# Optimization experiments

Hardware: AMD Instinct MI355X
Metric: run time of the kernel (lower is better)

## Reference

```python
import jax, jax.numpy as jnp
import numpy as np

ROPE_BASE = 10000.0


def _rope(x):
    # x: (B, S, H, D) -- rotate-half RoPE applied per head over the sequence dim
    B, S, H, D = x.shape
    half = D // 2
    inv_freq = 1.0 / (ROPE_BASE ** (jnp.arange(half, dtype=jnp.float32) / half))
    ang = jnp.arange(S, dtype=jnp.float32)[:, None] * inv_freq[None, :]  # (S, half)
    cos = jnp.cos(ang)[None, :, None, :].astype(x.dtype)
    sin = jnp.sin(ang)[None, :, None, :].astype(x.dtype)
    x1, x2 = x[..., :half], x[..., half:]
    return jnp.concatenate([x1 * cos - x2 * sin, x2 * cos + x1 * sin], axis=-1)


def setup_inputs() -> dict:
    key = jax.random.key(0)
    ks = jax.random.split(key, 7)
    B, S, D = 8, 1024, 512
    HD = 512  # num_heads * key_dim = 8 * 64
    scale = 0.02
    return {
        "query": jax.random.normal(ks[0], (B, S, D), dtype=jnp.float32),
        "value": jax.random.normal(ks[1], (B, S, D), dtype=jnp.float32),
        "key_in": jax.random.normal(ks[2], (B, S, D), dtype=jnp.float32),
        "Wq": jax.random.normal(ks[3], (D, HD), dtype=jnp.float32) * scale,
        "Wk": jax.random.normal(ks[4], (D, HD), dtype=jnp.float32) * scale,
        "Wv": jax.random.normal(ks[5], (D, HD), dtype=jnp.float32) * scale,
        "Wo": jax.random.normal(ks[6], (HD, D), dtype=jnp.float32) * scale,
    }


def reference(query, value, key_in, Wq, Wk, Wv, Wo):
    H, Dh = 8, 64
    B, Sq, _ = query.shape
    Sk = key_in.shape[1]
    # QKV projections, split heads: (B, S, H, Dh)
    q = (query @ Wq).reshape(B, Sq, H, Dh)
    v = (value @ Wv).reshape(B, Sk, H, Dh)
    k = (key_in @ Wk).reshape(B, Sk, H, Dh)
    # inline RoPE on q and k (applied before head transpose, as in the original)
    q = _rope(q)
    k = _rope(k)
    # scaled dot-product attention with causal mask
    q = q * (1.0 / jnp.sqrt(jnp.asarray(Dh, q.dtype)))
    scores = jnp.einsum("bqhd,bkhd->bhqk", q, k)  # (B, H, Sq, Sk)
    causal = jnp.tril(jnp.ones((Sq, Sk), dtype=bool))[None, None]
    scores = jnp.where(causal, scores, jnp.asarray(-1e9, scores.dtype))
    probs = jax.nn.softmax(scores, axis=-1)
    out = jnp.einsum("bhqk,bkhd->bqhd", probs, v)  # (B, Sq, H, Dh)
    out = out.reshape(B, Sq, H * Dh) @ Wo  # output projection
    return out
```

## Files before the change

kernel.cpp:

```cpp
#include <hip/hip_runtime.h>
#include <hip/hip_bf16.h>
#include <stdint.h>

#define DEV static __device__ __forceinline__

typedef __attribute__((ext_vector_type(8)))  short    s16x8;
typedef __attribute__((ext_vector_type(4)))  short    s16x4;
typedef __attribute__((ext_vector_type(8)))  __bf16   bf16x8;
typedef __attribute__((ext_vector_type(2)))  __bf16   bf16x2;
typedef __attribute__((ext_vector_type(4)))  float    f32x4;
typedef __attribute__((ext_vector_type(16))) float    f32x16;
typedef __attribute__((ext_vector_type(2)))  unsigned u32x2;
typedef __attribute__((ext_vector_type(4)))  unsigned u32x4;

DEV short f2b(float f){
  union{float f; uint32_t i;} x; x.f = f;
  uint32_t r = x.i + 0x7FFFu + ((x.i >> 16) & 1u);
  return (short)(r >> 16);
}
DEV unsigned packbf(float a, float b){
  bf16x2 v = { (__bf16)a, (__bf16)b };
  return __builtin_bit_cast(unsigned, v);
}
DEV bf16x8 as_bf(s16x8 v){ return __builtin_bit_cast(bf16x8, v); }
DEV float fexp2(float x){ return __builtin_amdgcn_exp2f(x); }
DEV f32x4 mf(s16x8 a, s16x8 b, f32x4 c){
  return __builtin_amdgcn_mfma_f32_16x16x32_bf16(as_bf(a), as_bf(b), c, 0, 0, 0);
}
DEV f32x16 mf32(s16x8 a, s16x8 b, f32x16 c){
  return __builtin_amdgcn_mfma_f32_32x32x16_bf16(as_bf(a), as_bf(b), c, 0, 0, 0);
}

DEV void gload_lds16(const void* g, void* l){
  __builtin_amdgcn_global_load_lds((const __attribute__((address_space(1))) void*)g,
                                   (__attribute__((address_space(3))) void*)l, 16, 0, 0);
}

#if __has_builtin(__builtin_amdgcn_permlane32_swap)
DEV void pswap2(unsigned a, unsigned b, unsigned& x, unsigned& y){
  u32x2 rr = __builtin_amdgcn_permlane32_swap(a, b, false, false);
  x = rr[0]; y = rr[1];
}
DEV float partner32(float v, int hi){
  unsigned u = __builtin_bit_cast(unsigned, v);
  u32x2 rr = __builtin_amdgcn_permlane32_swap(u, u, false, false);
  return __builtin_bit_cast(float, hi ? rr[0] : rr[1]);
}
#else
DEV void pswap2(unsigned a, unsigned b, unsigned& x, unsigned& y){
  unsigned pa_ = (unsigned)__shfl_xor((int)a, 32, 64);
  unsigned pb_ = (unsigned)__shfl_xor((int)b, 32, 64);
  int lo = ((threadIdx.x & 63) < 32);
  x = lo ? a   : pb_;
  y = lo ? pa_ : b;
}
DEV float partner32(float v, int hi){ (void)hi; return __shfl_xor(v, 32, 64); }
#endif

__global__ __launch_bounds__(256) void k_conv3(const float* __restrict__ q,
                                               const float* __restrict__ k,
                                               const float* __restrict__ v,
                                               short* __restrict__ out){
  int z = blockIdx.z;
  const float* in = (z == 0) ? q : (z == 1) ? k : v;
  int i = (blockIdx.x * 256 + threadIdx.x) * 4;
  float4 val = *(const float4*)(in + i);
  short o[4] = { f2b(val.x), f2b(val.y), f2b(val.z), f2b(val.w) };
  *(uint2*)(out + (size_t)z * 4194304 + i) = *(uint2*)o;
}

__global__ __launch_bounds__(256) void k_wt4(const float* __restrict__ w0,
                                             const float* __restrict__ w1,
                                             const float* __restrict__ w2,
                                             const float* __restrict__ w3,
                                             short* __restrict__ wt){
  __shared__ float tile[32][33];
  int z = blockIdx.z;
  const float* w = (z == 0) ? w0 : (z == 1) ? w1 : (z == 2) ? w2 : w3;
  short* o = wt + (size_t)z * 262144;
  int bx = blockIdx.x * 32, by = blockIdx.y * 32;
  int tx = threadIdx.x, ty = threadIdx.y;
  for (int j = 0; j < 32; j += 8)
    tile[ty + j][tx] = w[(size_t)(by + ty + j) * 512 + bx + tx];
  __syncthreads();
  for (int j = 0; j < 32; j += 8)
    o[(size_t)(bx + ty + j) * 512 + by + tx] = f2b(tile[tx][ty + j]);
}

__global__ __launch_bounds__(256) void k_table(float* __restrict__ tab){
  int idx = blockIdx.x * 256 + threadIdx.x;
  int s = idx >> 5, j = idx & 31;
  float inv = __expf(-(float)j * (1.0f / 32.0f) * logf(10000.0f));
  float ang = (float)s * inv;
  tab[idx * 2 + 0] = cosf(ang);
  tab[idx * 2 + 1] = sinf(ang);
}

__global__ __launch_bounds__(256) void k_qkv(const short* __restrict__ Xb,
                                             const short* __restrict__ Wcat,
                                             const float* __restrict__ tab,
                                             short* __restrict__ Qa,
                                             short* __restrict__ Ka,
                                             short* __restrict__ Vt){
  __shared__ __align__(16) short Al[2][4096];
  __shared__ __align__(16) short Bl[2][4096];
  const int t = threadIdx.x, w = t >> 6, lane = t & 63, fr = lane & 15, fg = lane >> 4;
  const int sel = blockIdx.y >> 2;
  const short* X = Xb + (size_t)sel * 4194304;
  const int bm = blockIdx.x * 128, bn = blockIdx.y * 128;
  const int wm = (w >> 1) * 64, wn = (w & 1) * 64;

  auto stage = [&](int buf, int k0){
#pragma unroll
    for (int q = 0; q < 2; q++){
      int lin = q * 256 + t;
      int row = lin >> 2, sl = lin & 3;
      int gs = (sl ^ (row & 3)) * 8;
      gload_lds16(X    + (size_t)(bm + row) * 512 + k0 + gs, &Al[buf][(q * 256 + w * 64) * 8]);
      gload_lds16(Wcat + (size_t)(bn + row) * 512 + k0 + gs, &Bl[buf][(q * 256 + w * 64) * 8]);
    }
  };

  f32x4 acc[4][4] = {};
  stage(0, 0);
  __syncthreads();
  int cur = 0;
  for (int t16 = 0; t16 < 16; ++t16){
    if (t16 < 15) stage(cur ^ 1, (t16 + 1) * 32);
    s16x8 af[4], bv[4];
#pragma unroll
    for (int f = 0; f < 4; f++){
      int ra = wm + f * 16 + fr;
      af[f] = *(const s16x8*)(&Al[cur][ra * 32 + ((fg ^ (ra & 3)) * 8)]);
      int rb = wn + f * 16 + fr;
      bv[f] = *(const s16x8*)(&Bl[cur][rb * 32 + ((fg ^ (rb & 3)) * 8)]);
    }
#pragma unroll
    for (int i = 0; i < 4; i++)
#pragma unroll
      for (int jj = 0; jj < 4; jj++)
        acc[i][jj] = mf(af[i], bv[jj], acc[i][jj]);
    __syncthreads();
    cur ^= 1;
  }

  const int row0 = bm + wm + fg * 4;
  const int b = row0 >> 10;
  const int s_base = row0 & 1023;
  const int hh = (((blockIdx.y & 3) * 128) + wn) >> 6;
  if (sel < 2){
    const float scale = (sel == 0) ? 0.125f * 1.44269504f : 1.0f;
    short* out = (sel == 0) ? Qa : Ka;
#pragma unroll
    for (int i = 0; i < 4; i++)
#pragma unroll
      for (int jj = 0; jj < 2; jj++){
        int d = jj * 16 + fr;
#pragma unroll
        for (int r = 0; r < 4; r++){
          int s = s_base + i * 16 + r;
          float2 cs = *(const float2*)(tab + (size_t)(s * 32 + d) * 2);
          float x1 = acc[i][jj][r], x2 = acc[i][jj + 2][r];
          size_t ob = ((size_t)((b * 8 + hh) * 1024 + s)) * 64 + d;
          out[ob]      = f2b((x1 * cs.x - x2 * cs.y) * scale);
          out[ob + 32] = f2b((x2 * cs.x + x1 * cs.y) * scale);
        }
      }
  } else {
#pragma unroll
    for (int i = 0; i < 4; i++)
#pragma unroll
      for (int jj = 0; jj < 4; jj++){
        int d = jj * 16 + fr;
        s16x4 pk;
#pragma unroll
        for (int r = 0; r < 4; r++) pk[r] = f2b(acc[i][jj][r]);
        size_t ob = ((size_t)((b * 8 + hh) * 64 + d)) * 1024 + s_base + i * 16;
        *(s16x4*)(Vt + ob) = pk;
      }
  }
}

__global__ __launch_bounds__(256) void k_attn(const short* __restrict__ Qb,
                                              const short* __restrict__ Kb,
                                              const short* __restrict__ Vt,
                                              short* __restrict__ O){
  __shared__ __align__(16) short KL[2][4096];
  __shared__ __align__(16) short VL[2][4096];
  const int bid = blockIdx.x;
  const int BiMap[8] = {7,6,5,4, 0,1,2,3};
  const int Bi = BiMap[bid >> 6];
  const int bh = bid & 63;
  const int B0 = Bi * 128;
  const int KVEND = B0 + 128;
  const int t = threadIdx.x, w = t >> 6, lane = t & 63;
  const int col = lane & 31, hi = lane >> 5;
  const short* Qp = Qb + (size_t)bh * 65536;
  const short* Kp = Kb + (size_t)bh * 65536;
  const short* Vp = Vt + (size_t)bh * 65536;
  const int qrow = B0 + 4 * col + w;

  s16x8 qb[4];
#pragma unroll
  for (int ks = 0; ks < 4; ks++)
    qb[ks] = *(const s16x8*)(Qp + (size_t)qrow * 64 + ks * 16 + hi * 8);

  int crow[16];
#pragma unroll
  for (int r = 0; r < 16; r++) crow[r] = (r & 3) + 8 * (r >> 2) + 4 * hi;

  f32x16 oacc[2] = {};
  float m = -1e30f, l = 0.f;

  auto stage = [&](int buf, int kv0){
#pragma unroll
    for (int R = 0; R < 2; R++){
      int lin = R * 256 + w * 64 + lane;
      int row = lin >> 3, slot = lin & 7;
      int gs = ((slot ^ (row & 7)) * 8);
      gload_lds16(Kp + (size_t)(kv0 + row) * 64 + gs, &KL[buf][(R * 256 + w * 64) * 8]);
      gload_lds16(Vp + (size_t)row * 1024 + kv0 + gs, &VL[buf][(R * 256 + w * 64) * 8]);
    }
  };

  stage(0, 0);
  __syncthreads();

  int cur = 0;
  for (int kv0 = 0; kv0 < KVEND; kv0 += 64){
    const bool hasNext = (kv0 + 64 < KVEND);
    if (hasNext) stage(cur ^ 1, kv0 + 64);
    __builtin_amdgcn_s_setprio(1);
    f32x16 sc[2];
#pragma unroll
    for (int f = 0; f < 2; f++){
      f32x16 s = {};
      int row = f * 32 + col, rx = row & 7;
#pragma unroll
      for (int ks = 0; ks < 4; ks++){
        s16x8 ka = *(const s16x8*)(&KL[cur][row * 64 + ((ks * 2 + hi) ^ rx) * 8]);
        s = mf32(ka, qb[ks], s);
      }
      sc[f] = s;
    }
    __builtin_amdgcn_s_setprio(0);
    if (kv0 >= B0){
#pragma unroll
      for (int f = 0; f < 2; f++)
#pragma unroll
        for (int r = 0; r < 16; r++){
          int kv = kv0 + f * 32 + crow[r];
          if (kv > qrow) sc[f][r] = -1e30f;
        }
    }
    float mx[16];
#pragma unroll
    for (int r = 0; r < 16; r++) mx[r] = fmaxf(sc[0][r], sc[1][r]);
#pragma unroll
    for (int off = 8; off >= 1; off >>= 1)
#pragma unroll
      for (int r = 0; r < off; r++) mx[r] = fmaxf(mx[r], mx[r + off]);
    float tm = fmaxf(mx[0], partner32(mx[0], hi));
    if (!__all(tm <= m + 8.f)){
      float mn = fmaxf(m, tm);
      float corr = fexp2(m - mn);
      m = mn;
      l *= corr;
      float cpv[16];
#pragma unroll
      for (int r = 0; r < 16; r++) cpv[r] = __shfl(corr, crow[r], 64);
#pragma unroll
      for (int r = 0; r < 16; r++){ oacc[0][r] *= cpv[r]; oacc[1][r] *= cpv[r]; }
    }
    float p[32];
#pragma unroll
    for (int f = 0; f < 2; f++)
#pragma unroll
      for (int i = 0; i < 16; i++) p[f * 16 + i] = fexp2(sc[f][i] - m);
    unsigned wq[2][8];
#pragma unroll
    for (int f = 0; f < 2; f++)
#pragma unroll
      for (int i = 0; i < 8; i++)
        wq[f][i] = packbf(p[f * 16 + 2 * i], p[f * 16 + 2 * i + 1]);
#pragma unroll
    for (int off = 16; off >= 1; off >>= 1)
#pragma unroll
      for (int r = 0; r < off; r++) p[r] += p[r + off];
    l += p[0] + partner32(p[0], hi);
    s16x8 pa[4];
#pragma unroll
    for (int f = 0; f < 2; f++)
#pragma unroll
      for (int half = 0; half < 2; half++){
        unsigned w0, w1, w2, w3;
        pswap2(wq[f][half * 4 + 0], wq[f][half * 4 + 2], w0, w2);
        pswap2(wq[f][half * 4 + 1], wq[f][half * 4 + 3], w1, w3);
        u32x4 uv = { w0, w1, w2, w3 };
        pa[f * 2 + half] = __builtin_bit_cast(s16x8, uv);
      }
    __builtin_amdgcn_s_setprio(1);
#pragma unroll
    for (int ks = 0; ks < 4; ks++)
#pragma unroll
      for (int df = 0; df < 2; df++){
        int row = df * 32 + col;
        s16x8 vb = *(const s16x8*)(&VL[cur][row * 64 + ((ks * 2 + hi) ^ (row & 7)) * 8]);
        oacc[df] = mf32(pa[ks], vb, oacc[df]);
      }
    __builtin_amdgcn_s_setprio(0);
    if (hasNext) __syncthreads();
    cur ^= 1;
  }

  const int b = bh >> 3, h = bh & 7;
  float lf[16];
#pragma unroll
  for (int r = 0; r < 16; r++) lf[r] = __shfl(l, crow[r], 64);
#pragma unroll
  for (int r = 0; r < 16; r++){
    int qq = B0 + 4 * crow[r] + w;
    float inv = 1.0f / lf[r];
    O[(size_t)(b * 1024 + qq) * 512 + h * 64 + col]      = f2b(oacc[0][r] * inv);
    O[(size_t)(b * 1024 + qq) * 512 + h * 64 + 32 + col] = f2b(oacc[1][r] * inv);
  }
}

__global__ __launch_bounds__(256, 2) void k_gemm_out(const short* __restrict__ X,
                                                     const short* __restrict__ Wt,
                                                     float* __restrict__ C){
  __shared__ __align__(16) short Al[2][8192];
  __shared__ __align__(16) short Bl[2][8192];
  const int t = threadIdx.x;
  const int w = t >> 6, lane = t & 63, fr = lane & 15, fg = lane >> 4;
  const int bm = blockIdx.x * 128, bn = blockIdx.y * 128;
  const int wm = (w >> 1) * 64, wn = (w & 1) * 64;

  auto stage = [&](int buf, int k0){
#pragma unroll
    for (int q = 0; q < 4; q++){
      int lin = q * 256 + t;
      int row = lin >> 3, sl = lin & 7;
      int gs = (sl ^ (row & 7)) * 8;
      gload_lds16(X  + (size_t)(bm + row) * 512 + k0 + gs, &Al[buf][(q * 256 + w * 64) * 8]);
      gload_lds16(Wt + (size_t)(bn + row) * 512 + k0 + gs, &Bl[buf][(q * 256 + w * 64) * 8]);
    }
  };

  f32x4 acc[4][4] = {};
  stage(0, 0);
  __syncthreads();
  int cur = 0;
  for (int t8 = 0; t8 < 8; ++t8){
    if (t8 < 7) stage(cur ^ 1, (t8 + 1) * 64);
#pragma unroll
    for (int kk = 0; kk < 2; kk++){
      s16x8 af[4], bv[4];
#pragma unroll
      for (int f = 0; f < 4; f++){
        int rowa = wm + f * 16 + fr;
        af[f] = *(const s16x8*)(&Al[cur][rowa * 64 + ((kk * 4 + fg) ^ (rowa & 7)) * 8]);
        int rowb = wn + f * 16 + fr;
        bv[f] = *(const s16x8*)(&Bl[cur][rowb * 64 + ((kk * 4 + fg) ^ (rowb & 7)) * 8]);
      }
#pragma unroll
      for (int i = 0; i < 4; i++)
#pragma unroll
        for (int jj = 0; jj < 4; jj++)
          acc[i][jj] = mf(af[i], bv[jj], acc[i][jj]);
    }
    __syncthreads();
    cur ^= 1;
  }
  const int row0 = bm + wm + fg * 4;
  const int col0 = bn + wn + fr;
#pragma unroll
  for (int i = 0; i < 4; i++)
#pragma unroll
    for (int jj = 0; jj < 4; jj++)
#pragma unroll
      for (int r = 0; r < 4; r++)
        C[(size_t)(row0 + i * 16 + r) * 512 + col0 + jj * 16] = acc[i][jj][r];
}

extern "C" void kernel_launch(void* const* d_in, const int* in_sizes, int n_in,
                              void* d_out, int out_size, void* d_ws, size_t ws_size,
                              hipStream_t stream){
  const float* query  = (const float*)d_in[0];
  const float* value  = (const float*)d_in[1];
  const float* key_in = (const float*)d_in[2];
  const float* Wq     = (const float*)d_in[3];
  const float* Wk     = (const float*)d_in[4];
  const float* Wv     = (const float*)d_in[5];
  const float* Wo     = (const float*)d_in[6];

  char* ws = (char*)d_ws;
  const size_t MB = 1ull << 20;
  short* Xb   = (short*)(ws);
  short* Wcat = (short*)(ws + 24 * MB);
  float* tab  = (float*)(ws + 26 * MB);
  short* Qa   = (short*)(ws + 26 * MB + 256 * 1024);
  short* Ka   = (short*)((char*)Qa + 8 * MB);
  short* Va   = (short*)((char*)Ka + 8 * MB);
  short* Oa   = Xb;
  short* Wot  = Wcat + 786432;

  k_conv3<<<dim3(4096, 1, 3), 256, 0, stream>>>(query, key_in, value, Xb);
  k_wt4<<<dim3(16, 16, 4), dim3(32, 8), 0, stream>>>(Wq, Wk, Wv, Wo, Wcat);
  k_table<<<128, 256, 0, stream>>>(tab);

  k_qkv<<<dim3(64, 12), 256, 0, stream>>>(Xb, Wcat, tab, Qa, Ka, Va);

  k_attn<<<512, 256, 0, stream>>>(Qa, Ka, Va, Oa);

  k_gemm_out<<<dim3(64, 4), 256, 0, stream>>>(Oa, Wot, (float*)d_out);
}
```

Measured before the change: 83.97 us.

## Switch to triple-buffered LDS pipeline with explicit vmcnt waits in all GEMM kernels

```diff
diff --git a/kernel.cpp b/kernel.cpp
--- a/kernel.cpp
+++ b/kernel.cpp
@@ -12,6 +12,10 @@
 typedef __attribute__((ext_vector_type(16))) float    f32x16;
 typedef __attribute__((ext_vector_type(2)))  unsigned u32x2;
 typedef __attribute__((ext_vector_type(4)))  unsigned u32x4;
+
+#define WAIT_VMCNT(N) do{ asm volatile("s_waitcnt vmcnt(" #N ")" ::: "memory"); \
+                          __builtin_amdgcn_sched_barrier(0); }while(0)
+DEV void barrier_raw(){ __builtin_amdgcn_sched_barrier(0); __builtin_amdgcn_s_barrier(); }
 
 DEV short f2b(float f){
   union{float f; uint32_t i;} x; x.f = f;
@@ -102,8 +106,8 @@
                                              short* __restrict__ Qa,
                                              short* __restrict__ Ka,
                                              short* __restrict__ Vt){
-  __shared__ __align__(16) short Al[2][4096];
-  __shared__ __align__(16) short Bl[2][4096];
+  __shared__ __align__(16) short Al[3][4096];
+  __shared__ __align__(16) short Bl[3][4096];
   const int t = threadIdx.x, w = t >> 6, lane = t & 63, fr = lane & 15, fg = lane >> 4;
   const int sel = blockIdx.y >> 2;
   const short* X = Xb + (size_t)sel * 4194304;
@@ -123,10 +127,14 @@
 
   f32x4 acc[4][4] = {};
   stage(0, 0);
-  __syncthreads();
-  int cur = 0;
+  stage(1, 32);
   for (int t16 = 0; t16 < 16; ++t16){
-    if (t16 < 15) stage(cur ^ 1, (t16 + 1) * 32);
+    barrier_raw();
+    int kc = t16 + 2; if (kc > 15) kc = 15;
+    stage((t16 + 2) % 3, kc * 32);
+    WAIT_VMCNT(8);
+    barrier_raw();
+    const int cur = t16 % 3;
     s16x8 af[4], bv[4];
 #pragma unroll
     for (int f = 0; f < 4; f++){
@@ -140,8 +148,6 @@
 #pragma unroll
       for (int jj = 0; jj < 4; jj++)
         acc[i][jj] = mf(af[i], bv[jj], acc[i][jj]);
-    __syncthreads();
-    cur ^= 1;
   }
 
   const int row0 = bm + wm + fg * 4;
@@ -185,14 +191,14 @@
                                               const short* __restrict__ Kb,
                                               const short* __restrict__ Vt,
                                               short* __restrict__ O){
-  __shared__ __align__(16) short KL[2][4096];
-  __shared__ __align__(16) short VL[2][4096];
+  __shared__ __align__(16) short KL[3][4096];
+  __shared__ __align__(16) short VL[3][4096];
   const int bid = blockIdx.x;
   const int BiMap[8] = {7,6,5,4, 0,1,2,3};
   const int Bi = BiMap[bid >> 6];
   const int bh = bid & 63;
   const int B0 = Bi * 128;
-  const int KVEND = B0 + 128;
+  const int nch = (B0 >> 6) + 2;
   const int t = threadIdx.x, w = t >> 6, lane = t & 63;
   const int col = lane & 31, hi = lane >> 5;
   const short* Qp = Qb + (size_t)bh * 65536;
@@ -224,12 +230,16 @@
   };
 
   stage(0, 0);
-  __syncthreads();
-
-  int cur = 0;
-  for (int kv0 = 0; kv0 < KVEND; kv0 += 64){
-    const bool hasNext = (kv0 + 64 < KVEND);
-    if (hasNext) stage(cur ^ 1, kv0 + 64);
+  stage(1, (nch > 1 ? 64 : 0));
+
+  for (int i = 0; i < nch; ++i){
+    const int kv0 = i * 64;
+    barrier_raw();
+    int kc = i + 2; if (kc > nch - 1) kc = nch - 1;
+    stage((i + 2) % 3, kc * 64);
+    WAIT_VMCNT(8);
+    barrier_raw();
+    const int cur = i % 3;
     __builtin_amdgcn_s_setprio(1);
     f32x16 sc[2];
 #pragma unroll
@@ -276,13 +286,13 @@
 #pragma unroll
     for (int f = 0; f < 2; f++)
 #pragma unroll
-      for (int i = 0; i < 16; i++) p[f * 16 + i] = fexp2(sc[f][i] - m);
+      for (int i2 = 0; i2 < 16; i2++) p[f * 16 + i2] = fexp2(sc[f][i2] - m);
     unsigned wq[2][8];
 #pragma unroll
     for (int f = 0; f < 2; f++)
 #pragma unroll
-      for (int i = 0; i < 8; i++)
-        wq[f][i] = packbf(p[f * 16 + 2 * i], p[f * 16 + 2 * i + 1]);
+      for (int i2 = 0; i2 < 8; i2++)
+        wq[f][i2] = packbf(p[f * 16 + 2 * i2], p[f * 16 + 2 * i2 + 1]);
 #pragma unroll
     for (int off = 16; off >= 1; off >>= 1)
 #pragma unroll
@@ -309,8 +319,6 @@
         oacc[df] = mf32(pa[ks], vb, oacc[df]);
       }
     __builtin_amdgcn_s_setprio(0);
-    if (hasNext) __syncthreads();
-    cur ^= 1;
   }
 
   const int b = bh >> 3, h = bh & 7;
@@ -326,11 +334,11 @@
   }
 }
 
-__global__ __launch_bounds__(256, 2) void k_gemm_out(const short* __restrict__ X,
-                                                     const short* __restrict__ Wt,
-                                                     float* __restrict__ C){
-  __shared__ __align__(16) short Al[2][8192];
-  __shared__ __align__(16) short Bl[2][8192];
+__global__ __launch_bounds__(256) void k_gemm_out(const short* __restrict__ X,
+                                                  const short* __restrict__ Wt,
+                                                  float* __restrict__ C){
+  __shared__ __align__(16) short Al[3][8192];
+  __shared__ __align__(16) short Bl[3][8192];
   const int t = threadIdx.x;
   const int w = t >> 6, lane = t & 63, fr = lane & 15, fg = lane >> 4;
   const int bm = blockIdx.x * 128, bn = blockIdx.y * 128;
@@ -349,10 +357,14 @@
 
   f32x4 acc[4][4] = {};
   stage(0, 0);
-  __syncthreads();
-  int cur = 0;
+  stage(1, 64);
   for (int t8 = 0; t8 < 8; ++t8){
-    if (t8 < 7) stage(cur ^ 1, (t8 + 1) * 64);
+    barrier_raw();
+    int kc = t8 + 2; if (kc > 7) kc = 7;
+    stage((t8 + 2) % 3, kc * 64);
+    WAIT_VMCNT(16);
+    barrier_raw();
+    const int cur = t8 % 3;
 #pragma unroll
     for (int kk = 0; kk < 2; kk++){
       s16x8 af[4], bv[4];
@@ -369,8 +381,6 @@
         for (int jj = 0; jj < 4; jj++)
           acc[i][jj] = mf(af[i], bv[jj], acc[i][jj]);
     }
-    __syncthreads();
-    cur ^= 1;
   }
   const int row0 = bm + wm + fg * 4;
   const int col0 = bn + wn + fr;
```

Result: faster. 80.99 us (-3.5%).
